# Kernel tuning notes

Measured on AMD Instinct MI355X. Metric: run time of the kernel, lower is better.

Reference implementation:

```python
import jax, jax.numpy as jnp
import numpy as np

B, C, H, W = 8, 512, 64, 64
HEADS, GROUPS, EPS = 4, 32, 1e-5


def setup_inputs() -> dict:
    key = jax.random.key(0)
    ks = jax.random.split(key, 7)
    s = 0.02
    return {
        "x": jax.random.normal(ks[0], (B, C, H, W), dtype=jnp.float32),
        "gn_w": jnp.ones((C,), dtype=jnp.float32),
        "gn_b": jnp.zeros((C,), dtype=jnp.float32),
        "qkv_w": jax.random.normal(ks[1], (3 * C, C), dtype=jnp.float32) * s,
        "qkv_b": jnp.zeros((3 * C,), dtype=jnp.float32),
        "proj_w": jax.random.normal(ks[2], (C, C), dtype=jnp.float32) * s,
        "proj_b": jnp.zeros((C,), dtype=jnp.float32),
    }


def reference(x, gn_w, gn_b, qkv_w, qkv_b, proj_w, proj_b):
    b, c, h, w = x.shape
    d = c // HEADS  # per-head channel dim
    n = h * w
    # GroupNorm(32, C)
    xg = x.reshape(b, GROUPS, -1)
    mu = xg.mean(axis=-1, keepdims=True)
    var = xg.var(axis=-1, keepdims=True)
    hn = ((xg - mu) * jax.lax.rsqrt(var + EPS)).reshape(b, c, h, w)
    hn = hn * gn_w[:, None, None] + gn_b[:, None, None]
    # 1x1 conv qkv: [3C, C] contraction over channels
    qkv = jnp.einsum('oc,bchw->bohw', qkv_w, hn) + qkv_b[:, None, None]
    qkv = qkv.reshape(b, 3, HEADS, d, n)
    q, k, v = qkv[:, 0], qkv[:, 1], qkv[:, 2]  # each [b, heads, d, n]
    # NOTE: as in the source, q @ k^T contracts over spatial dim -> [b,heads,d,d]
    attn = jnp.einsum('bhdn,bhen->bhde', q, k) * (d ** -0.5)
    attn = jax.nn.softmax(attn, axis=-1)
    out = jnp.einsum('bhde,bhen->bhdn', attn, v).reshape(b, c, h, w)
    out = jnp.einsum('oc,bchw->bohw', proj_w, out) + proj_b[:, None, None]
    return x + out
```

## Files before the change

### kernel.cpp

```cpp
#include <hip/hip_runtime.h>
#include <hip/hip_bf16.h>

typedef __hip_bfloat16 bf16;
typedef __bf16 v8bf __attribute__((ext_vector_type(8)));
typedef float  v4f  __attribute__((ext_vector_type(4)));

struct __align__(8) bf16x4 { bf16 x, y, z, w; };

__device__ __forceinline__ bf16 f2b(float v) { return __float2bfloat16(v); }

#define NSP 4096
#define CCH 512

__device__ __forceinline__ void async_cp16(const bf16* g, __bf16* l) {
    __builtin_amdgcn_global_load_lds(
        (const __attribute__((address_space(1))) unsigned int*)(unsigned long long)g,
        (__attribute__((address_space(3))) unsigned int*)(unsigned int)(unsigned long long)l,
        16, 0, 0);
}

__global__ __launch_bounds__(256) void wconv_kernel(const float* __restrict__ src,
                                                    bf16* __restrict__ dst, int n4) {
    int i = blockIdx.x * 256 + threadIdx.x;
    if (i < n4) {
        float4 v = ((const float4*)src)[i];
        bf16x4 o = { f2b(v.x), f2b(v.y), f2b(v.z), f2b(v.w) };
        ((bf16x4*)dst)[i] = o;
    }
}

__global__ __launch_bounds__(256) void gn_stats_kernel(const float* __restrict__ x,
                                                       float* __restrict__ stats) {
    int blk = blockIdx.x;
    int b = blk >> 5, g = blk & 31;
    size_t base = ((size_t)(b * CCH + g * 16)) * NSP;
    const float4* xp4 = (const float4*)(x + base);
    int t = threadIdx.x;
    float s = 0.f, s2 = 0.f;
    for (int i = t; i < 16384; i += 256) {
        float4 v = xp4[i];
        s  += v.x + v.y + v.z + v.w;
        s2 += v.x * v.x + v.y * v.y + v.z * v.z + v.w * v.w;
    }
    for (int off = 32; off > 0; off >>= 1) {
        s  += __shfl_down(s, off);
        s2 += __shfl_down(s2, off);
    }
    __shared__ float red[8];
    int wid = t >> 6, lid = t & 63;
    if (lid == 0) { red[wid] = s; red[wid + 4] = s2; }
    __syncthreads();
    if (t == 0) {
        float ts  = red[0] + red[1] + red[2] + red[3];
        float ts2 = red[4] + red[5] + red[6] + red[7];
        float mean = ts * (1.f / 65536.f);
        float var  = ts2 * (1.f / 65536.f) - mean * mean;
        stats[blk * 2]     = mean;
        stats[blk * 2 + 1] = rsqrtf(var + 1e-5f);
    }
}

__global__ __launch_bounds__(256) void gn_norm_t_kernel(const float* __restrict__ x,
                                                        const float* __restrict__ gw,
                                                        const float* __restrict__ gb,
                                                        const float* __restrict__ stats,
                                                        bf16* __restrict__ hnT) {
    __shared__ float sT[64][65];
    int n0 = blockIdx.x * 64, c0 = blockIdx.y * 64, b = blockIdx.z;
    int t = threadIdx.x;
    int cl = t >> 4, nl4 = (t & 15) << 2;
#pragma unroll
    for (int it = 0; it < 4; ++it) {
        int crow = cl + it * 16;
        int c = c0 + crow;
        int bg = b * 32 + (c >> 4);
        float mean = stats[bg * 2], rstd = stats[bg * 2 + 1];
        float wsc = gw[c] * rstd;
        float bb  = gb[c] - mean * wsc;
        float4 v = *(const float4*)&x[((long)b * CCH + c) * NSP + n0 + nl4];
        sT[crow][nl4 + 0] = v.x * wsc + bb;
        sT[crow][nl4 + 1] = v.y * wsc + bb;
        sT[crow][nl4 + 2] = v.z * wsc + bb;
        sT[crow][nl4 + 3] = v.w * wsc + bb;
    }
    __syncthreads();
    int nl = t >> 4, cl4 = (t & 15) << 2;
#pragma unroll
    for (int it = 0; it < 4; ++it) {
        int nrow = nl + it * 16;
        bf16x4 ov = { f2b(sT[cl4 + 0][nrow]), f2b(sT[cl4 + 1][nrow]),
                      f2b(sT[cl4 + 2][nrow]), f2b(sT[cl4 + 3][nrow]) };
        *(bf16x4*)&hnT[((long)b * NSP + n0 + nrow) * CCH + c0 + cl4] = ov;
    }
}

__device__ __forceinline__ void gemm_core(const bf16* __restrict__ A, long as,
                                          const bf16* __restrict__ B, long bs,
                                          int K, v4f acc[4][4],
                                          __bf16* sA, __bf16* sB) {
    int t = threadIdx.x;
    int lane = t & 63, wv = t >> 6;
    int wr = wv >> 1, wc = wv & 1;
    int lq = lane & 15, quad = lane >> 4;
    int r0 = wv * 16 + (lane >> 2);
    int koff = (lane & 3) * 8;
    __bf16* ldsA0 = sA + wv * 512 + lane * 8;
    __bf16* ldsA1 = ldsA0 + 2048;
    __bf16* ldsB0 = sB + wv * 512 + lane * 8;
    __bf16* ldsB1 = ldsB0 + 2048;
    const __bf16* aBase = sA + (wr * 64) * 32;
    const __bf16* bBase = sB + (wc * 64) * 32;

    for (int k0 = 0; k0 < K; k0 += 32) {
        __syncthreads();
        async_cp16(A + (long)r0 * as + k0 + koff,        ldsA0);
        async_cp16(A + (long)(r0 + 64) * as + k0 + koff, ldsA1);
        async_cp16(B + (long)r0 * bs + k0 + koff,        ldsB0);
        async_cp16(B + (long)(r0 + 64) * bs + k0 + koff, ldsB1);
        __syncthreads();
        v8bf a[4], bf[4];
#pragma unroll
        for (int i = 0; i < 4; ++i)
            a[i] = *(const v8bf*)(aBase + (i * 16 + lq) * 32 + quad * 8);
#pragma unroll
        for (int j = 0; j < 4; ++j)
            bf[j] = *(const v8bf*)(bBase + (j * 16 + lq) * 32 + quad * 8);
#pragma unroll
        for (int i = 0; i < 4; ++i)
#pragma unroll
            for (int j = 0; j < 4; ++j)
                acc[i][j] = __builtin_amdgcn_mfma_f32_16x16x32_bf16(a[i], bf[j], acc[i][j], 0, 0, 0);
    }
}

__device__ __forceinline__ void gemm256_core(const bf16* __restrict__ A, long lda,
                                             const bf16* __restrict__ B, long ldb,
                                             int K, v4f acc[8][4], char* sLds) {
    const int t = threadIdx.x;
    const int lane = t & 63, wv = t >> 6;
    const int wm = wv >> 2, wn = wv & 3;
    const int lq = lane & 15, quad = lane >> 4;
    const int xsw = (lq & 7) << 4;
    const int kq0 = ((quad << 4)) ^ xsw;
    const int kq1 = (64 | (quad << 4)) ^ xsw;
    const int aRow0 = (wm * 128 + lq) << 7;
    const int bRow0 = (wn * 64 + lq) << 7;
    const int NT = K >> 6;

    auto STAGE = [&](const bf16* mb, long ld, int ldsbyte, int ktile, int h) {
#pragma unroll
        for (int s = 0; s < 2; ++s) {
            int L = (s << 13) + (t << 4);
            int row = L >> 7;
            int kb = (L & 127) ^ ((row & 7) << 4);
            const char* g = (const char*)(mb + (long)(h * 128 + row) * ld + (long)ktile * 64);
            async_cp16((const bf16*)(g + kb),
                       (__bf16*)(sLds + ldsbyte + (h << 14) + L));
        }
    };

    STAGE(B, ldb, 32768, 0, 0);
    STAGE(B, ldb, 32768, 0, 1);
    STAGE(A, lda, 0,     0, 0);
    STAGE(A, lda, 0,     0, 1);
    if (NT > 1) {
        STAGE(B, ldb, 65536 + 32768, 1, 0);
        STAGE(B, ldb, 65536 + 32768, 1, 1);
        asm volatile("s_waitcnt vmcnt(4)" ::: "memory");
    } else {
        asm volatile("s_waitcnt vmcnt(0)" ::: "memory");
    }
    __builtin_amdgcn_s_barrier();
    asm volatile("" ::: "memory");

    for (int kt = 0; kt < NT; ++kt) {
        const int cb = (kt & 1) << 16;
        const int nb = cb ^ 65536;
        const int bufA = cb, bufB = cb | 32768;
        v8bf a[4][2], b0[2][2], b1[2][2];

#pragma unroll
        for (int ii = 0; ii < 4; ++ii) {
            a[ii][0] = *(const v8bf*)(sLds + bufA + aRow0 + ((ii * 16) << 7) + kq0);
            a[ii][1] = *(const v8bf*)(sLds + bufA + aRow0 + ((ii * 16) << 7) + kq1);
        }
#pragma unroll
        for (int jj = 0; jj < 2; ++jj) {
            b0[jj][0] = *(const v8bf*)(sLds + bufB + bRow0 + ((jj * 16) << 7) + kq0);
            b0[jj][1] = *(const v8bf*)(sLds + bufB + bRow0 + ((jj * 16) << 7) + kq1);
        }
        if (kt + 1 < NT) STAGE(A, lda, nb, kt + 1, 0);
        __builtin_amdgcn_s_barrier();
        asm volatile("s_waitcnt lgkmcnt(0)" ::: "memory");
        __builtin_amdgcn_sched_barrier(0);
        __builtin_amdgcn_s_setprio(1);
#pragma unroll
        for (int ii = 0; ii < 4; ++ii)
#pragma unroll
            for (int jj = 0; jj < 2; ++jj) {
                acc[ii][jj] = __builtin_amdgcn_mfma_f32_16x16x32_bf16(a[ii][0], b0[jj][0], acc[ii][jj], 0, 0, 0);
                acc[ii][jj] = __builtin_amdgcn_mfma_f32_16x16x32_bf16(a[ii][1], b0[jj][1], acc[ii][jj], 0, 0, 0);
            }
        __builtin_amdgcn_s_setprio(0);
        __builtin_amdgcn_s_barrier();
        asm volatile("" ::: "memory");

#pragma unroll
        for (int jj = 0; jj < 2; ++jj) {
            b1[jj][0] = *(const v8bf*)(sLds + bufB + bRow0 + ((32 + jj * 16) << 7) + kq0);
            b1[jj][1] = *(const v8bf*)(sLds + bufB + bRow0 + ((32 + jj * 16) << 7) + kq1);
        }
        if (kt + 1 < NT) STAGE(A, lda, nb, kt + 1, 1);
        __builtin_amdgcn_s_barrier();
        asm volatile("s_waitcnt lgkmcnt(0)" ::: "memory");
        __builtin_amdgcn_sched_barrier(0);
        __builtin_amdgcn_s_setprio(1);
#pragma unroll
        for (int ii = 0; ii < 4; ++ii)
#pragma unroll
            for (int jj = 0; jj < 2; ++jj) {
                acc[ii][2 + jj] = __builtin_amdgcn_mfma_f32_16x16x32_bf16(a[ii][0], b1[jj][0], acc[ii][2 + jj], 0, 0, 0);
                acc[ii][2 + jj] = __builtin_amdgcn_mfma_f32_16x16x32_bf16(a[ii][1], b1[jj][1], acc[ii][2 + jj], 0, 0, 0);
            }
        __builtin_amdgcn_s_setprio(0);
        __builtin_amdgcn_s_barrier();
        asm volatile("" ::: "memory");

#pragma unroll
        for (int ii = 0; ii < 4; ++ii) {
            a[ii][0] = *(const v8bf*)(sLds + bufA + aRow0 + ((64 + ii * 16) << 7) + kq0);
            a[ii][1] = *(const v8bf*)(sLds + bufA + aRow0 + ((64 + ii * 16) << 7) + kq1);
        }
        if (kt + 2 < NT) STAGE(B, ldb, bufB, kt + 2, 0);
        __builtin_amdgcn_s_barrier();
        asm volatile("s_waitcnt lgkmcnt(0)" ::: "memory");
        __builtin_amdgcn_sched_barrier(0);
        __builtin_amdgcn_s_setprio(1);
#pragma unroll
        for (int ii = 0; ii < 4; ++ii)
#pragma unroll
            for (int jj = 0; jj < 2; ++jj) {
                acc[4 + ii][2 + jj] = __builtin_amdgcn_mfma_f32_16x16x32_bf16(a[ii][0], b1[jj][0], acc[4 + ii][2 + jj], 0, 0, 0);
                acc[4 + ii][2 + jj] = __builtin_amdgcn_mfma_f32_16x16x32_bf16(a[ii][1], b1[jj][1], acc[4 + ii][2 + jj], 0, 0, 0);
            }
        __builtin_amdgcn_s_setprio(0);
        __builtin_amdgcn_s_barrier();
        asm volatile("" ::: "memory");

        if (kt + 2 < NT) STAGE(B, ldb, bufB, kt + 2, 1);
        __builtin_amdgcn_s_barrier();
        __builtin_amdgcn_s_setprio(1);
#pragma unroll
        for (int ii = 0; ii < 4; ++ii)
#pragma unroll
            for (int jj = 0; jj < 2; ++jj) {
                acc[4 + ii][jj] = __builtin_amdgcn_mfma_f32_16x16x32_bf16(a[ii][0], b0[jj][0], acc[4 + ii][jj], 0, 0, 0);
                acc[4 + ii][jj] = __builtin_amdgcn_mfma_f32_16x16x32_bf16(a[ii][1], b0[jj][1], acc[4 + ii][jj], 0, 0, 0);
            }
        __builtin_amdgcn_s_setprio(0);
        if (kt + 2 < NT) asm volatile("s_waitcnt vmcnt(4)" ::: "memory");
        else             asm volatile("s_waitcnt vmcnt(0)" ::: "memory");
        __builtin_amdgcn_s_barrier();
        asm volatile("" ::: "memory");
    }
}

__global__ __launch_bounds__(512, 2) void qkv_gemm_kernel(const bf16* __restrict__ hnT,
                                                          const bf16* __restrict__ qkv_wb,
                                                          const float* __restrict__ qkv_b,
                                                          bf16* __restrict__ qkbuf,
                                                          bf16* __restrict__ vT) {
    __shared__ __align__(16) char sLds[131072];
    int n0 = blockIdx.x * 256, o0 = blockIdx.y * 256, b = blockIdx.z;
    v4f acc[8][4] = {};
    gemm256_core(hnT + ((long)b * NSP + n0) * CCH, CCH,
                 qkv_wb + (long)o0 * CCH, CCH, CCH, acc, sLds);
    int t = threadIdx.x, lane = t & 63, wv = t >> 6, wm = wv >> 2, wn = wv & 3;
    int lq = lane & 15, quad = lane >> 4;
    if (o0 < 1024) {
#pragma unroll
        for (int j = 0; j < 4; ++j) {
            int o = o0 + wn * 64 + j * 16 + lq;
            float bias = qkv_b[o];
#pragma unroll
            for (int i = 0; i < 8; ++i) {
                int n = n0 + wm * 128 + i * 16 + quad * 4;
                v4f v = acc[i][j];
                bf16x4 ov = { f2b(v[0] + bias), f2b(v[1] + bias),
                              f2b(v[2] + bias), f2b(v[3] + bias) };
                *(bf16x4*)&qkbuf[((long)b * 1024 + o) * NSP + n] = ov;
            }
        }
    } else {
#pragma unroll
        for (int j = 0; j < 4; ++j) {
            int e = o0 - 1024 + wn * 64 + j * 16 + lq;
            float bias = qkv_b[1024 + e];
#pragma unroll
            for (int i = 0; i < 8; ++i) {
                int n = n0 + wm * 128 + i * 16 + quad * 4;
                v4f v = acc[i][j];
#pragma unroll
                for (int r = 0; r < 4; ++r)
                    vT[((long)b * NSP + n + r) * CCH + e] = f2b(v[r] + bias);
            }
        }
    }
}

__global__ __launch_bounds__(256) void qk_gemm_kernel(const bf16* __restrict__ qkbuf,
                                                      float* __restrict__ P_part) {
    __shared__ __align__(16) __bf16 sA[128 * 32];
    __shared__ __align__(16) __bf16 sB[128 * 32];
    int s = blockIdx.x, bh = blockIdx.y;
    int b = bh >> 2, h = bh & 3;
    const bf16* q  = qkbuf + ((long)b * 1024 + h * 128) * NSP + s * 512;
    const bf16* kk = qkbuf + ((long)b * 1024 + 512 + h * 128) * NSP + s * 512;
    v4f acc[4][4] = {};
    gemm_core(q, NSP, kk, NSP, 512, acc, sA, sB);
    float* Pp = P_part + ((long)s * 32 + bh) * 16384;
    int t = threadIdx.x, lane = t & 63, wv = t >> 6, wr = wv >> 1, wc = wv & 1;
    int lq = lane & 15, quad = lane >> 4;
#pragma unroll
    for (int j = 0; j < 4; ++j) {
        int e = wc * 64 + j * 16 + lq;
#pragma unroll
        for (int i = 0; i < 4; ++i) {
            int d = wr * 64 + i * 16 + quad * 4;
            v4f v = acc[i][j];
#pragma unroll
            for (int r = 0; r < 4; ++r) Pp[(long)(d + r) * 128 + e] = v[r];
        }
    }
}

__global__ __launch_bounds__(128) void softmax_kernel(const float* __restrict__ P_part,
                                                      bf16* __restrict__ Pb) {
    int row = blockIdx.x;
    int bh = row >> 7, d = row & 127;
    int t = threadIdx.x;
    float v = 0.f;
#pragma unroll
    for (int s = 0; s < 8; ++s)
        v += P_part[((long)s * 32 + bh) * 16384 + (long)d * 128 + t];
    v *= 0.08838834764831845f;
    float m = v;
    for (int off = 32; off > 0; off >>= 1) m = fmaxf(m, __shfl_down(m, off));
    __shared__ float sm[2];
    if ((t & 63) == 0) sm[t >> 6] = m;
    __syncthreads();
    m = fmaxf(sm[0], sm[1]);
    float e = __expf(v - m);
    float ssum = e;
    for (int off = 32; off > 0; off >>= 1) ssum += __shfl_down(ssum, off);
    __shared__ float ss[2];
    if ((t & 63) == 0) ss[t >> 6] = ssum;
    __syncthreads();
    ssum = ss[0] + ss[1];
    Pb[(long)row * 128 + t] = f2b(e / ssum);
}

__global__ __launch_bounds__(256) void pv_gemm_kernel(const bf16* __restrict__ Pb,
                                                      const bf16* __restrict__ vT,
                                                      bf16* __restrict__ attT) {
    __shared__ __align__(16) __bf16 sA[128 * 32];
    __shared__ __align__(16) __bf16 sB[128 * 32];
    int n0 = blockIdx.x * 128, bh = blockIdx.y;
    int b = bh >> 2, h = bh & 3;
    v4f acc[4][4] = {};
    gemm_core(Pb + (long)bh * 16384, 128,
              vT + ((long)b * NSP + n0) * CCH + h * 128, CCH, 128, acc, sA, sB);
    int t = threadIdx.x, lane = t & 63, wv = t >> 6, wr = wv >> 1, wc = wv & 1;
    int lq = lane & 15, quad = lane >> 4;
#pragma unroll
    for (int j = 0; j < 4; ++j) {
        int n = n0 + wc * 64 + j * 16 + lq;
#pragma unroll
        for (int i = 0; i < 4; ++i) {
            int d = wr * 64 + i * 16 + quad * 4;
            v4f v = acc[i][j];
            bf16x4 ov = { f2b(v[0]), f2b(v[1]), f2b(v[2]), f2b(v[3]) };
            *(bf16x4*)&attT[((long)b * NSP + n) * CCH + h * 128 + d] = ov;
        }
    }
}

__global__ __launch_bounds__(512, 2) void proj_gemm_kernel(const bf16* __restrict__ attT,
                                                           const bf16* __restrict__ proj_wb,
                                                           const float* __restrict__ proj_b,
                                                           const float* __restrict__ x,
                                                           float* __restrict__ out) {
    __shared__ __align__(16) char sLds[131072];
    int n0 = blockIdx.x * 256, c0 = blockIdx.y * 256, b = blockIdx.z;
    v4f acc[8][4] = {};
    gemm256_core(attT + ((long)b * NSP + n0) * CCH, CCH,
                 proj_wb + (long)c0 * CCH, CCH, CCH, acc, sLds);
    int t = threadIdx.x, lane = t & 63, wv = t >> 6, wm = wv >> 2, wn = wv & 3;
    int lq = lane & 15, quad = lane >> 4;
#pragma unroll
    for (int j = 0; j < 4; ++j) {
        int c = c0 + wn * 64 + j * 16 + lq;
        float bias = proj_b[c];
#pragma unroll
        for (int i = 0; i < 8; ++i) {
            int n = n0 + wm * 128 + i * 16 + quad * 4;
            long idx = ((long)b * CCH + c) * NSP + n;
            float4 r = *(const float4*)&x[idx];
            v4f v = acc[i][j];
            float4 ov = { v[0] + bias + r.x, v[1] + bias + r.y,
                          v[2] + bias + r.z, v[3] + bias + r.w };
            *(float4*)&out[idx] = ov;
        }
    }
}

extern "C" void kernel_launch(void* const* d_in, const int* in_sizes, int n_in,
                              void* d_out, int out_size, void* d_ws, size_t ws_size,
                              hipStream_t stream) {
    const float* x      = (const float*)d_in[0];
    const float* gn_w   = (const float*)d_in[1];
    const float* gn_b   = (const float*)d_in[2];
    const float* qkv_w  = (const float*)d_in[3];
    const float* qkv_b  = (const float*)d_in[4];
    const float* proj_w = (const float*)d_in[5];
    const float* proj_b = (const float*)d_in[6];
    float* out = (float*)d_out;

    char* ws = (char*)d_ws;
    bf16*  hnT    = (bf16*)ws;
    float* P_part = (float*)ws;
    bf16*  attT   = (bf16*)ws;
    bf16*  qkbuf  = (bf16*)(ws + 33554432);
    bf16*  vT     = (bf16*)(ws + 100663296);
    bf16*  Pb     = (bf16*)(ws + 134217728);
    float* stats  = (float*)(ws + 135266304);
    bf16*  qkv_wb = (bf16*)(ws + 135270400);
    bf16*  proj_wb= (bf16*)(ws + 136843264);

    wconv_kernel<<<768, 256, 0, stream>>>(qkv_w, qkv_wb, 196608);
    wconv_kernel<<<256, 256, 0, stream>>>(proj_w, proj_wb, 65536);
    gn_stats_kernel<<<256, 256, 0, stream>>>(x, stats);
    gn_norm_t_kernel<<<dim3(64, 8, 8), 256, 0, stream>>>(x, gn_w, gn_b, stats, hnT);
    qkv_gemm_kernel<<<dim3(16, 6, 8), 512, 0, stream>>>(hnT, qkv_wb, qkv_b, qkbuf, vT);
    qk_gemm_kernel<<<dim3(8, 32), 256, 0, stream>>>(qkbuf, P_part);
    softmax_kernel<<<4096, 128, 0, stream>>>(P_part, Pb);
    pv_gemm_kernel<<<dim3(32, 32), 256, 0, stream>>>(Pb, vT, attT);
    proj_gemm_kernel<<<dim3(16, 2, 8), 512, 0, stream>>>(attT, proj_wb, proj_b, x, out);
}
```

Before: 305.5 us.

## Rewrite PV GEMM with register-resident P and swizzled async V loads; drop barriers

The PV kernel now holds the 128x128 P tile for each head in registers. It streams two 128-row V tiles per block into XOR-swizzled LDS with async global-to-LDS copies, which halves the grid and double-buffers the second tile under the first tile's MFMAs. Separately, the shared 256x256 GEMM core used by the qkv and proj GEMMs drops several s_barrier, lgkmcnt-wait and sched_barrier calls between its MFMA phases to cut synchronisation stalls. The barrier removal relies on compiler-inserted waits and on buffer separation being enough for correctness, so it risks LDS races if any stage overlaps.

Result: no change. 307.4 us (+0.6%).

```diff
diff --git a/kernel.cpp b/kernel.cpp
--- a/kernel.cpp
+++ b/kernel.cpp
@@ -190,9 +190,6 @@
             b0[jj][1] = *(const v8bf*)(sLds + bufB + bRow0 + ((jj * 16) << 7) + kq1);
         }
         if (kt + 1 < NT) STAGE(A, lda, nb, kt + 1, 0);
-        __builtin_amdgcn_s_barrier();
-        asm volatile("s_waitcnt lgkmcnt(0)" ::: "memory");
-        __builtin_amdgcn_sched_barrier(0);
         __builtin_amdgcn_s_setprio(1);
 #pragma unroll
         for (int ii = 0; ii < 4; ++ii)
@@ -211,9 +208,6 @@
             b1[jj][1] = *(const v8bf*)(sLds + bufB + bRow0 + ((32 + jj * 16) << 7) + kq1);
         }
         if (kt + 1 < NT) STAGE(A, lda, nb, kt + 1, 1);
-        __builtin_amdgcn_s_barrier();
-        asm volatile("s_waitcnt lgkmcnt(0)" ::: "memory");
-        __builtin_amdgcn_sched_barrier(0);
         __builtin_amdgcn_s_setprio(1);
 #pragma unroll
         for (int ii = 0; ii < 4; ++ii)
@@ -232,9 +226,6 @@
             a[ii][1] = *(const v8bf*)(sLds + bufA + aRow0 + ((64 + ii * 16) << 7) + kq1);
         }
         if (kt + 2 < NT) STAGE(B, ldb, bufB, kt + 2, 0);
-        __builtin_amdgcn_s_barrier();
-        asm volatile("s_waitcnt lgkmcnt(0)" ::: "memory");
-        __builtin_amdgcn_sched_barrier(0);
         __builtin_amdgcn_s_setprio(1);
 #pragma unroll
         for (int ii = 0; ii < 4; ++ii)
@@ -248,7 +239,6 @@
         asm volatile("" ::: "memory");
 
         if (kt + 2 < NT) STAGE(B, ldb, bufB, kt + 2, 1);
-        __builtin_amdgcn_s_barrier();
         __builtin_amdgcn_s_setprio(1);
 #pragma unroll
         for (int ii = 0; ii < 4; ++ii)
@@ -363,24 +353,69 @@
 __global__ __launch_bounds__(256) void pv_gemm_kernel(const bf16* __restrict__ Pb,
                                                       const bf16* __restrict__ vT,
                                                       bf16* __restrict__ attT) {
-    __shared__ __align__(16) __bf16 sA[128 * 32];
-    __shared__ __align__(16) __bf16 sB[128 * 32];
-    int n0 = blockIdx.x * 128, bh = blockIdx.y;
+    __shared__ __align__(16) char sV[2][32768];
+    int ng = blockIdx.x, bh = blockIdx.y;
     int b = bh >> 2, h = bh & 3;
-    v4f acc[4][4] = {};
-    gemm_core(Pb + (long)bh * 16384, 128,
-              vT + ((long)b * NSP + n0) * CCH + h * 128, CCH, 128, acc, sA, sB);
     int t = threadIdx.x, lane = t & 63, wv = t >> 6, wr = wv >> 1, wc = wv & 1;
     int lq = lane & 15, quad = lane >> 4;
-#pragma unroll
-    for (int j = 0; j < 4; ++j) {
-        int n = n0 + wc * 64 + j * 16 + lq;
-#pragma unroll
-        for (int i = 0; i < 4; ++i) {
-            int d = wr * 64 + i * 16 + quad * 4;
-            v4f v = acc[i][j];
-            bf16x4 ov = { f2b(v[0]), f2b(v[1]), f2b(v[2]), f2b(v[3]) };
-            *(bf16x4*)&attT[((long)b * NSP + n) * CCH + h * 128 + d] = ov;
+
+    auto STAGEV = [&](int n0, int buf) {
+#pragma unroll
+        for (int s = 0; s < 8; ++s) {
+            int L = (s << 12) + (t << 4);
+            int row = L >> 8;
+            int col = (L & 255) ^ ((row & 7) << 4);
+            async_cp16((const bf16*)((const char*)(vT + ((long)b * NSP + n0 + row) * CCH + h * 128) + col),
+                       (__bf16*)(&sV[buf][0] + L));
+        }
+    };
+
+    int n00 = ng * 256;
+    STAGEV(n00, 0);
+    v8bf a[4][4];
+    const char* Pp = (const char*)(Pb + (long)bh * 16384);
+#pragma unroll
+    for (int i = 0; i < 4; ++i)
+#pragma unroll
+        for (int ks = 0; ks < 4; ++ks)
+            a[i][ks] = *(const v8bf*)(Pp + ((wr * 64 + i * 16 + lq) << 8) + (ks << 6) + (quad << 4));
+    STAGEV(n00 + 128, 1);
+    asm volatile("s_waitcnt vmcnt(8)" ::: "memory");
+    __syncthreads();
+
+#pragma unroll
+    for (int nt = 0; nt < 2; ++nt) {
+        int n0 = n00 + nt * 128;
+        const char* base = &sV[nt][0];
+        v4f acc[4][4] = {};
+#pragma unroll
+        for (int ks = 0; ks < 4; ++ks) {
+            v8bf bv[4];
+#pragma unroll
+            for (int j = 0; j < 4; ++j) {
+                int r = wc * 64 + j * 16 + lq;
+                bv[j] = *(const v8bf*)(base + (r << 8) + (((ks << 6) + (quad << 4)) ^ ((r & 7) << 4)));
+            }
+#pragma unroll
+            for (int i = 0; i < 4; ++i)
+#pragma unroll
+                for (int j = 0; j < 4; ++j)
+                    acc[i][j] = __builtin_amdgcn_mfma_f32_16x16x32_bf16(a[i][ks], bv[j], acc[i][j], 0, 0, 0);
+        }
+#pragma unroll
+        for (int j = 0; j < 4; ++j) {
+            int n = n0 + wc * 64 + j * 16 + lq;
+#pragma unroll
+            for (int i = 0; i < 4; ++i) {
+                int d = wr * 64 + i * 16 + quad * 4;
+                v4f v = acc[i][j];
+                bf16x4 ov = { f2b(v[0]), f2b(v[1]), f2b(v[2]), f2b(v[3]) };
+                *(bf16x4*)&attT[((long)b * NSP + n) * CCH + h * 128 + d] = ov;
+            }
+        }
+        if (nt == 0) {
+            asm volatile("s_waitcnt vmcnt(0)" ::: "memory");
+            __syncthreads();
         }
     }
 }
@@ -444,6 +479,6 @@
     qkv_gemm_kernel<<<dim3(16, 6, 8), 512, 0, stream>>>(hnT, qkv_wb, qkv_b, qkbuf, vT);
     qk_gemm_kernel<<<dim3(8, 32), 256, 0, stream>>>(qkbuf, P_part);
     softmax_kernel<<<4096, 128, 0, stream>>>(P_part, Pb);
-    pv_gemm_kernel<<<dim3(32, 32), 256, 0, stream>>>(Pb, vT, attT);
+    pv_gemm_kernel<<<dim3(16, 32), 256, 0, stream>>>(Pb, vT, attT);
     proj_gemm_kernel<<<dim3(16, 2, 8), 512, 0, stream>>>(attT, proj_wb, proj_b, x, out);
 }
```
